# Optimization experiments

Hardware: AMD Instinct MI355X
Metric: run time of the kernel (lower is better)

The kernel has to match this reference:

```python
import jax, jax.numpy as jnp
import numpy as np

EXPERTS, IN_DIM, OUT_DIM, BATCH = 8, 1024, 1024, 16384

def setup_inputs() -> dict:
    key = jax.random.key(0)
    k1, k2, k3, k4 = jax.random.split(key, 4)
    bound = np.sqrt(6.0 / (IN_DIM * OUT_DIM)).astype(np.float32)
    bbound = np.sqrt(6.0 / (1 * OUT_DIM)).astype(np.float32)
    return {
        "x": jax.random.normal(k1, (BATCH, IN_DIM), dtype=jnp.float32),
        "weights": jax.random.uniform(k2, (BATCH, EXPERTS), dtype=jnp.float32),
        "W": jax.random.uniform(k3, (EXPERTS, IN_DIM, OUT_DIM), jnp.float32, -bound, bound),
        "b": jax.random.uniform(k4, (EXPERTS, 1, OUT_DIM), jnp.float32, -bbound, bbound),
    }

def reference(x, weights, W, b):
    # y[b,o] = sum_e weights[b,e] * (x[b,:] @ W[e] + b[e])
    # Fused triple einsum avoids materializing the [B,E,O] intermediate.
    y = jnp.einsum("be,bi,eio->bo", weights, x, W)
    y = y + jnp.einsum("be,eo->bo", weights, b[:, 0, :])
    return y
```

## Files before the change

### kernel.cpp

```cpp
#include <hip/hip_runtime.h>
#include <hip/hip_bf16.h>
#include <stdint.h>

#define BATCH   16384
#define EXPERTS 8
#define IN_DIM  1024
#define OUT_DIM 1024

typedef unsigned short u16;
typedef short  bf16x8 __attribute__((ext_vector_type(8)));
typedef float  f32x4  __attribute__((ext_vector_type(4)));

__device__ __forceinline__ u16 f2bf(float f) {
  uint32_t u = __float_as_uint(f);
  u += 0x7fffu + ((u >> 16) & 1u);
  return (u16)(u >> 16);
}

#define GLDS16(g, l)                                                      \
  __builtin_amdgcn_global_load_lds(                                       \
      (const __attribute__((address_space(1))) void*)(g),                 \
      (__attribute__((address_space(3))) void*)(l), 16, 0, 0)

#define MFMA_BF16 __builtin_amdgcn_mfma_f32_16x16x32_bf16
#define SB0 __builtin_amdgcn_sched_barrier(0)
#define LGKM(N) asm volatile("s_waitcnt lgkmcnt(" #N ")" ::: "memory")

__global__ void cvt_x(const float* __restrict__ x, u16* __restrict__ xb) {
  size_t i = ((size_t)blockIdx.x * 256 + threadIdx.x) * 4;
  float4 v = *reinterpret_cast<const float4*>(x + i);
  ushort4 o;
  o.x = f2bf(v.x); o.y = f2bf(v.y); o.z = f2bf(v.z); o.w = f2bf(v.w);
  *reinterpret_cast<ushort4*>(xb + i) = o;
}

__global__ void cvt_w(const float* __restrict__ W, u16* __restrict__ wbt) {
  __shared__ u16 t[64][72];
  const int e  = blockIdx.z;
  const int i0 = blockIdx.x * 64;
  const int o0 = blockIdx.y * 64;
  const int tid = threadIdx.x;
  const int c  = (tid & 15) * 4;
  const int r_ = tid >> 4;
  const float* src = W + ((size_t)e << 20);
#pragma unroll
  for (int p = 0; p < 4; ++p) {
    int r = r_ + p * 16;
    float4 v = *reinterpret_cast<const float4*>(src + (size_t)(i0 + r) * 1024 + o0 + c);
    t[r][c + 0] = f2bf(v.x); t[r][c + 1] = f2bf(v.y);
    t[r][c + 2] = f2bf(v.z); t[r][c + 3] = f2bf(v.w);
  }
  __syncthreads();
  u16* dst = wbt + ((size_t)e << 20);
#pragma unroll
  for (int p = 0; p < 4; ++p) {
    int orow = r_ + p * 16;
    ushort4 u;
    u.x = t[c + 0][orow]; u.y = t[c + 1][orow];
    u.z = t[c + 2][orow]; u.w = t[c + 3][orow];
    *reinterpret_cast<ushort4*>(dst + (size_t)(o0 + orow) * 1024 + i0 + c) = u;
  }
}

__global__ __launch_bounds__(512, 2)
void zgemm(const u16* __restrict__ xb, const u16* __restrict__ wbt,
           const float* __restrict__ wts, const float* __restrict__ bias,
           float* __restrict__ y) {
  __shared__ u16 sm[69632];
  char* smb = (char*)sm;
  float* rl = (float*)(sm + 65536);

  const int tid = threadIdx.x;
  const int l   = tid & 63;
  const int w   = tid >> 6;
  const int wm  = w >> 2;
  const int wn  = w & 3;
  const int x8  = blockIdx.x & 7;
  const int jj  = blockIdx.x >> 3;
  const int n0  = (x8 >> 1) * 256;
  const int b0  = (((x8 & 1) << 5) + jj) << 8;

#pragma unroll
  for (int i = 0; i < 4; ++i) {
    const int flat = tid + i * 512;
    const int e = flat & 7, r = flat >> 3;
    const float* wr = wts + (size_t)(b0 + r) * EXPERTS;
    float we = fmaxf(wr[e], 1e-20f);
    float rr = (e < 7) ? we / fmaxf(wr[e + 1], 1e-20f) : we;
    rl[e * 256 + r] = rr;
  }

  const int rb    = (w << 3) + (l >> 3);
  const int chunk = ((l & 7) ^ (l >> 3)) << 3;
  const u16* pAg = xb  + (size_t)(b0 + rb) * IN_DIM + chunk;
  const u16* pBg = wbt + (size_t)(n0 + rb) * 1024 + chunk;

  const int l15  = l & 15;
  const int kb0  = (((l >> 4) << 4)) ^ ((l & 7) << 4);
  const int arow = (wm * 128 + l15) * 128;
  const int brow = (wn * 64 + l15) * 128;
  const int wlo  = (wm << 9) + ((l >> 4) << 4);

  f32x4 acc[8][4];
#pragma unroll
  for (int m = 0; m < 8; ++m)
#pragma unroll
    for (int n = 0; n < 4; ++n) acc[m][n] = (f32x4){0.f, 0.f, 0.f, 0.f};

#define STG_A(q, dstE, ev_kv)                                              \
  GLDS16(pAg + (size_t)((q) * 64) * 1024 + (ev_kv),                        \
         sm + (dstE) + (q) * 4096 + (w << 9))
#define STG_B(q, dstE, off)                                                \
  GLDS16(pBg + (off) + (size_t)((q) * 64) * 1024,                          \
         sm + (dstE) + (q) * 4096 + (w << 9))

  STG_A(0, 0, 0); STG_A(1, 0, 0); STG_A(2, 0, 0); STG_A(3, 0, 0);
  STG_B(0, 32768, 0); STG_B(1, 32768, 0); STG_B(2, 32768, 0); STG_B(3, 32768, 0);
  asm volatile("s_waitcnt vmcnt(0)" ::: "memory");
  LGKM(0);
  __builtin_amdgcn_s_barrier();

#define MM(AV, BV, MB)                                                     \
  __builtin_amdgcn_s_setprio(1);                                           \
  _Pragma("unroll")                                                        \
  for (int m = 0; m < 4; ++m)                                              \
    _Pragma("unroll")                                                      \
    for (int n = 0; n < 4; ++n)                                            \
      acc[(MB) + m][n] = MFMA_BF16(AV[m], BV[n], acc[(MB) + m][n], 0, 0, 0); \
  __builtin_amdgcn_s_setprio(0);

#pragma unroll 1
  for (int t = 0; t < 128; ++t) {
    const int tn  = (t + 1) & 127;
    const int e1  = tn >> 4, k1 = tn & 15;
    const int ArB = (t & 1) << 15;
    const int AwE = ((t + 1) & 1) << 14;
    const int BrB = 65536 + ((t & 1) << 15);
    const int BwE = 32768 + (((t + 1) & 1) << 14);
    const size_t aoffg = (size_t)k1 * 64;
    const size_t boffg = (size_t)e1 * 1048576 + (size_t)k1 * 64;

    bf16x8 a0[4], b0v[4], a1[4], a2v[4], b1v[4], a3[4];

#pragma unroll
    for (int m = 0; m < 4; ++m)
      a0[m] = *(const bf16x8*)(smb + ArB + arow + m * 2048 + kb0);
#pragma unroll
    for (int n = 0; n < 4; ++n)
      b0v[n] = *(const bf16x8*)(smb + BrB + brow + n * 2048 + kb0);
#pragma unroll
    for (int m = 0; m < 4; ++m)
      a1[m] = *(const bf16x8*)(smb + ArB + arow + (m + 4) * 2048 + kb0);
    STG_A(0, AwE, aoffg); STG_A(1, AwE, aoffg);
    STG_A(2, AwE, aoffg); STG_A(3, AwE, aoffg);
    STG_B(0, BwE, boffg); STG_B(1, BwE, boffg);
    STG_B(2, BwE, boffg); STG_B(3, BwE, boffg);

    LGKM(4); SB0;
#pragma unroll
    for (int m = 0; m < 4; ++m)
      a2v[m] = *(const bf16x8*)(smb + ArB + arow + m * 2048 + (kb0 ^ 64));
#pragma unroll
    for (int n = 0; n < 4; ++n)
      b1v[n] = *(const bf16x8*)(smb + BrB + brow + n * 2048 + (kb0 ^ 64));
    MM(a0, b0v, 0)

    LGKM(8); SB0;
#pragma unroll
    for (int m = 0; m < 4; ++m)
      a3[m] = *(const bf16x8*)(smb + ArB + arow + (m + 4) * 2048 + (kb0 ^ 64));
    MM(a1, b0v, 4)

    LGKM(4); SB0;
    MM(a2v, b1v, 0)

    LGKM(0); SB0;
    MM(a3, b1v, 4)

    asm volatile("s_waitcnt vmcnt(0)" ::: "memory");
    __builtin_amdgcn_s_barrier();

    if ((t & 15) == 15 && t != 127) {
      const int e = t >> 4;
#pragma unroll
      for (int m = 0; m < 8; ++m) {
        const f32x4 rv = *(const f32x4*)(smb + 131072 + e * 1024 + wlo + m * 64);
#pragma unroll
        for (int n = 0; n < 4; ++n) acc[m][n] *= rv;
      }
      LGKM(0); SB0;
    }
  }
  asm volatile("s_waitcnt vmcnt(0)" ::: "memory");

  float bv[4][8];
#pragma unroll
  for (int n = 0; n < 4; ++n) {
    const int c = n0 + wn * 64 + n * 16 + l15;
#pragma unroll
    for (int ee = 0; ee < 8; ++ee) bv[n][ee] = bias[ee * OUT_DIM + c];
  }
#pragma unroll
  for (int m = 0; m < 8; ++m) {
    const f32x4 rv7 = *(const f32x4*)(smb + 131072 + 7 * 1024 + wlo + m * 64);
    const int r0 = b0 + wm * 128 + m * 16 + ((l >> 4) << 2);
#pragma unroll
    for (int j = 0; j < 4; ++j) {
      const float* wr = wts + (size_t)(r0 + j) * EXPERTS;
      float w8[8];
#pragma unroll
      for (int ee = 0; ee < 8; ++ee) w8[ee] = wr[ee];
#pragma unroll
      for (int n = 0; n < 4; ++n) {
        const int c = n0 + wn * 64 + n * 16 + l15;
        float v = acc[m][n][j] * rv7[j];
#pragma unroll
        for (int ee = 0; ee < 8; ++ee) v += w8[ee] * bv[n][ee];
        y[(size_t)(r0 + j) * OUT_DIM + c] = v;
      }
    }
  }
}

extern "C" void kernel_launch(void* const* d_in, const int* in_sizes, int n_in,
                              void* d_out, int out_size, void* d_ws, size_t ws_size,
                              hipStream_t stream) {
  const float* x    = (const float*)d_in[0];
  const float* wts  = (const float*)d_in[1];
  const float* W    = (const float*)d_in[2];
  const float* bias = (const float*)d_in[3];
  float* y = (float*)d_out;

  const size_t xb_elems = (size_t)BATCH * IN_DIM;
  const size_t wb_elems = (size_t)EXPERTS * IN_DIM * OUT_DIM;
  if (ws_size < (xb_elems + wb_elems) * sizeof(u16)) return;
  u16* xb  = (u16*)d_ws;
  u16* wbt = xb + xb_elems;

  cvt_x<<<(BATCH * IN_DIM) / (4 * 256), 256, 0, stream>>>(x, xb);
  cvt_w<<<dim3(IN_DIM / 64, OUT_DIM / 64, EXPERTS), 256, 0, stream>>>(W, wbt);
  zgemm<<<dim3(256), 512, 0, stream>>>(xb, wbt, wts, bias, y);
}
```

Baseline: 259.7 us.

## Unroll main loop by two with constant buffer offsets and remap tile grid

Unrolls the K/expert loop by two so the double-buffer read and write offsets become compile-time constants. It changes the block-to-tile mapping so consecutive blocks share the same batch rows and cover all four N tiles, which should improve L2 reuse of the x tiles. It also batches the LDS loads of the ratio vectors before applying the rescale. The cost is a larger code body and different L2 locality for the weight tiles.

```diff
diff --git a/kernel.cpp b/kernel.cpp
--- a/kernel.cpp
+++ b/kernel.cpp
@@ -25,6 +25,7 @@
 #define MFMA_BF16 __builtin_amdgcn_mfma_f32_16x16x32_bf16
 #define SB0 __builtin_amdgcn_sched_barrier(0)
 #define LGKM(N) asm volatile("s_waitcnt lgkmcnt(" #N ")" ::: "memory")
+#define VM0     asm volatile("s_waitcnt vmcnt(0)" ::: "memory")
 
 __global__ void cvt_x(const float* __restrict__ x, u16* __restrict__ xb) {
   size_t i = ((size_t)blockIdx.x * 256 + threadIdx.x) * 4;
@@ -77,8 +78,8 @@
   const int wn  = w & 3;
   const int x8  = blockIdx.x & 7;
   const int jj  = blockIdx.x >> 3;
-  const int n0  = (x8 >> 1) * 256;
-  const int b0  = (((x8 & 1) << 5) + jj) << 8;
+  const int b0  = ((x8 << 3) + (jj >> 2)) << 8;
+  const int n0  = (jj & 3) << 8;
 
 #pragma unroll
   for (int i = 0; i < 4; ++i) {
@@ -90,10 +91,10 @@
     rl[e * 256 + r] = rr;
   }
 
-  const int rb    = (w << 3) + (l >> 3);
+  const int rbl   = (w << 3) + (l >> 3);
   const int chunk = ((l & 7) ^ (l >> 3)) << 3;
-  const u16* pAg = xb  + (size_t)(b0 + rb) * IN_DIM + chunk;
-  const u16* pBg = wbt + (size_t)(n0 + rb) * 1024 + chunk;
+  const u16* pAg = xb  + (size_t)(b0 + rbl) * IN_DIM + chunk;
+  const u16* pBg = wbt + (size_t)(n0 + rbl) * 1024 + chunk;
 
   const int l15  = l & 15;
   const int kb0  = (((l >> 4) << 4)) ^ ((l & 7) << 4);
@@ -107,19 +108,13 @@
 #pragma unroll
     for (int n = 0; n < 4; ++n) acc[m][n] = (f32x4){0.f, 0.f, 0.f, 0.f};
 
-#define STG_A(q, dstE, ev_kv)                                              \
-  GLDS16(pAg + (size_t)((q) * 64) * 1024 + (ev_kv),                        \
+#define STG_A(q, dstE, kv)                                                 \
+  GLDS16(pAg + (size_t)((q) * 64) * 1024 + (size_t)(kv) * 64,              \
          sm + (dstE) + (q) * 4096 + (w << 9))
 #define STG_B(q, dstE, off)                                                \
   GLDS16(pBg + (off) + (size_t)((q) * 64) * 1024,                          \
          sm + (dstE) + (q) * 4096 + (w << 9))
 
-  STG_A(0, 0, 0); STG_A(1, 0, 0); STG_A(2, 0, 0); STG_A(3, 0, 0);
-  STG_B(0, 32768, 0); STG_B(1, 32768, 0); STG_B(2, 32768, 0); STG_B(3, 32768, 0);
-  asm volatile("s_waitcnt vmcnt(0)" ::: "memory");
-  LGKM(0);
-  __builtin_amdgcn_s_barrier();
-
 #define MM(AV, BV, MB)                                                     \
   __builtin_amdgcn_s_setprio(1);                                           \
   _Pragma("unroll")                                                        \
@@ -129,69 +124,69 @@
       acc[(MB) + m][n] = MFMA_BF16(AV[m], BV[n], acc[(MB) + m][n], 0, 0, 0); \
   __builtin_amdgcn_s_setprio(0);
 
+  STG_A(0, 0, 0); STG_A(1, 0, 0); STG_A(2, 0, 0); STG_A(3, 0, 0);
+  STG_B(0, 32768, 0); STG_B(1, 32768, 0); STG_B(2, 32768, 0); STG_B(3, 32768, 0);
+  VM0;
+  LGKM(0);
+  __builtin_amdgcn_s_barrier();
+
+#define BODY(TT, ARB, BRB, AWE, BWE)                                       \
+  {                                                                        \
+    const int tn  = ((TT) + 1) & 127;                                      \
+    const int e1  = tn >> 4, k1 = tn & 15;                                 \
+    const size_t boffg = (size_t)e1 * 1048576 + (size_t)k1 * 64;           \
+    bf16x8 a0[4], b0v[4], a1[4], a2v[4], b1v[4], a3[4];                    \
+    _Pragma("unroll")                                                      \
+    for (int m = 0; m < 4; ++m)                                            \
+      a0[m] = *(const bf16x8*)(smb + (ARB) + arow + m * 2048 + kb0);       \
+    _Pragma("unroll")                                                      \
+    for (int n = 0; n < 4; ++n)                                            \
+      b0v[n] = *(const bf16x8*)(smb + (BRB) + brow + n * 2048 + kb0);      \
+    _Pragma("unroll")                                                      \
+    for (int m = 0; m < 4; ++m)                                            \
+      a1[m] = *(const bf16x8*)(smb + (ARB) + arow + (m + 4) * 2048 + kb0); \
+    STG_A(0, AWE, k1); STG_A(1, AWE, k1); STG_A(2, AWE, k1); STG_A(3, AWE, k1); \
+    STG_B(0, BWE, boffg); STG_B(1, BWE, boffg);                            \
+    STG_B(2, BWE, boffg); STG_B(3, BWE, boffg);                            \
+    LGKM(4); SB0;                              \
+    _Pragma("unroll")                                                      \
+    for (int m = 0; m < 4; ++m)                                            \
+      a2v[m] = *(const bf16x8*)(smb + (ARB) + arow + m * 2048 + (kb0 ^ 64)); \
+    _Pragma("unroll")                                                      \
+    for (int n = 0; n < 4; ++n)                                            \
+      b1v[n] = *(const bf16x8*)(smb + (BRB) + brow + n * 2048 + (kb0 ^ 64)); \
+    MM(a0, b0v, 0)                                                 \
+    LGKM(8); SB0;                                             \
+    _Pragma("unroll")                                                      \
+    for (int m = 0; m < 4; ++m)                                            \
+      a3[m] = *(const bf16x8*)(smb + (ARB) + arow + (m + 4) * 2048 + (kb0 ^ 64)); \
+    MM(a1, b0v, 4)                                                 \
+    LGKM(4); SB0;                                             \
+    MM(a2v, b1v, 0)                                                \
+    LGKM(0); SB0;                                             \
+    MM(a3, b1v, 4)                                                 \
+    VM0;                                           \
+    __builtin_amdgcn_s_barrier();              \
+    if (((TT) & 15) == 15 && (TT) != 127) {                                \
+      const int e = (TT) >> 4;                                             \
+      f32x4 rv[8];                                                         \
+      _Pragma("unroll")                                                    \
+      for (int m = 0; m < 8; ++m)                                          \
+        rv[m] = *(const f32x4*)(smb + 131072 + e * 1024 + wlo + m * 64);   \
+      LGKM(0); SB0;                                                        \
+      _Pragma("unroll")                                                    \
+      for (int m = 0; m < 8; ++m)                                          \
+        _Pragma("unroll")                                                  \
+        for (int n = 0; n < 4; ++n) acc[m][n] *= rv[m];                    \
+    }                                                                      \
+  }
+
 #pragma unroll 1
-  for (int t = 0; t < 128; ++t) {
-    const int tn  = (t + 1) & 127;
-    const int e1  = tn >> 4, k1 = tn & 15;
-    const int ArB = (t & 1) << 15;
-    const int AwE = ((t + 1) & 1) << 14;
-    const int BrB = 65536 + ((t & 1) << 15);
-    const int BwE = 32768 + (((t + 1) & 1) << 14);
-    const size_t aoffg = (size_t)k1 * 64;
-    const size_t boffg = (size_t)e1 * 1048576 + (size_t)k1 * 64;
-
-    bf16x8 a0[4], b0v[4], a1[4], a2v[4], b1v[4], a3[4];
-
-#pragma unroll
-    for (int m = 0; m < 4; ++m)
-      a0[m] = *(const bf16x8*)(smb + ArB + arow + m * 2048 + kb0);
-#pragma unroll
-    for (int n = 0; n < 4; ++n)
-      b0v[n] = *(const bf16x8*)(smb + BrB + brow + n * 2048 + kb0);
-#pragma unroll
-    for (int m = 0; m < 4; ++m)
-      a1[m] = *(const bf16x8*)(smb + ArB + arow + (m + 4) * 2048 + kb0);
-    STG_A(0, AwE, aoffg); STG_A(1, AwE, aoffg);
-    STG_A(2, AwE, aoffg); STG_A(3, AwE, aoffg);
-    STG_B(0, BwE, boffg); STG_B(1, BwE, boffg);
-    STG_B(2, BwE, boffg); STG_B(3, BwE, boffg);
-
-    LGKM(4); SB0;
-#pragma unroll
-    for (int m = 0; m < 4; ++m)
-      a2v[m] = *(const bf16x8*)(smb + ArB + arow + m * 2048 + (kb0 ^ 64));
-#pragma unroll
-    for (int n = 0; n < 4; ++n)
-      b1v[n] = *(const bf16x8*)(smb + BrB + brow + n * 2048 + (kb0 ^ 64));
-    MM(a0, b0v, 0)
-
-    LGKM(8); SB0;
-#pragma unroll
-    for (int m = 0; m < 4; ++m)
-      a3[m] = *(const bf16x8*)(smb + ArB + arow + (m + 4) * 2048 + (kb0 ^ 64));
-    MM(a1, b0v, 4)
-
-    LGKM(4); SB0;
-    MM(a2v, b1v, 0)
-
-    LGKM(0); SB0;
-    MM(a3, b1v, 4)
-
-    asm volatile("s_waitcnt vmcnt(0)" ::: "memory");
-    __builtin_amdgcn_s_barrier();
-
-    if ((t & 15) == 15 && t != 127) {
-      const int e = t >> 4;
-#pragma unroll
-      for (int m = 0; m < 8; ++m) {
-        const f32x4 rv = *(const f32x4*)(smb + 131072 + e * 1024 + wlo + m * 64);
-#pragma unroll
-        for (int n = 0; n < 4; ++n) acc[m][n] *= rv;
-      }
-      LGKM(0); SB0;
-    }
-  }
-  asm volatile("s_waitcnt vmcnt(0)" ::: "memory");
+  for (int t = 0; t < 128; t += 2) {
+    BODY(t,     0,     65536, 16384, 49152)
+    BODY(t + 1, 32768, 98304, 0,     32768)
+  }
+  VM0; LGKM(0);
 
   float bv[4][8];
 #pragma unroll
```

After: 243.8 us. 6.1% less time.
